# Kernel optimization log

Hardware: AMD Instinct MI355X
Metric: run time of the kernel (lower is better)

## Reference

```python
import jax, jax.numpy as jnp
import numpy as np

B, S, IN_DIM = 2, 2048, 1024
DIMS, QH, KVH = 1024, 16, 4
HD = DIMS // QH          # head_dims = 64
G = QH // KVH            # groups = 4


def setup_inputs() -> dict:
    key = jax.random.key(0)
    k1, k2, k3, k4, k5, k6 = jax.random.split(key, 6)
    scale = 0.02
    q_in = jax.random.normal(k1, (B, S, IN_DIM), dtype=jnp.float32)
    kv_in = jax.random.normal(k2, (B, S, IN_DIM), dtype=jnp.float32)
    # causal mask (True = attend)
    mask = jnp.tril(jnp.ones((S, S), dtype=bool))
    Wq = jax.random.normal(k3, (IN_DIM, QH, HD), dtype=jnp.float32) * scale
    Wk = jax.random.normal(k4, (IN_DIM, KVH, HD), dtype=jnp.float32) * scale
    Wv = jax.random.normal(k5, (IN_DIM, KVH, HD), dtype=jnp.float32) * scale
    Wo = jax.random.normal(k6, (KVH * HD, IN_DIM), dtype=jnp.float32) * scale
    return {"q_in": q_in, "kv_in": kv_in, "mask": mask,
            "Wq": Wq, "Wk": Wk, "Wv": Wv, "Wo": Wo}


def reference(q_in, kv_in, mask, Wq, Wk, Wv, Wo):
    b, s, _ = q_in.shape
    # projections (DenseGeneral, no bias)
    q = jnp.einsum('bsi,ihd->bshd', q_in, Wq)   # [B,S,QH,HD]
    k = jnp.einsum('bsi,ihd->bshd', kv_in, Wk)  # [B,S,KVH,HD]
    v = jnp.einsum('bsi,ihd->bshd', kv_in, Wv)  # [B,S,KVH,HD]
    # rearrange '... s (h g) d -> ... g h s d' with g=G (h outer, g inner),
    # then einsum '... g h s d, ... h a d -> ... h s a' sums over g.
    # Equivalent (and cheaper): sum q over the group axis first.
    q_g = q.reshape(b, s, KVH, G, HD).sum(axis=3)        # [B,S,KVH,HD]
    q_g = jnp.transpose(q_g, (0, 2, 1, 3))               # [B,KVH,S,HD]
    k = jnp.transpose(k, (0, 2, 1, 3))                   # [B,KVH,S,HD]
    v = jnp.transpose(v, (0, 2, 1, 3))                   # [B,KVH,S,HD]
    scores = jnp.einsum('bhsd,bhad->bhsa', q_g, k)       # [B,KVH,S,S]
    scores = jnp.where(mask[None, None, :, :], scores, -jnp.inf)
    attn = jax.nn.softmax(scores / (HD ** 0.5), axis=-1)
    out = jnp.einsum('bhsa,bhad->bhsd', attn, v)         # [B,KVH,S,HD]
    out = jnp.transpose(out, (0, 2, 1, 3)).reshape(b, s, KVH * HD)
    return out @ Wo                                      # [B,S,IN_DIM]
```

## Files before the change

kernel.cpp:

```cpp
#include <hip/hip_runtime.h>
#include <hip/hip_bf16.h>

#define SS 2048

typedef __attribute__((ext_vector_type(8))) short bf16x8;
typedef __attribute__((ext_vector_type(4))) float f32x4;

__device__ __forceinline__ short f2bf(float f){
    unsigned u = __float_as_uint(f);
    u += 0x7fff + ((u >> 16) & 1);
    return (short)(u >> 16);
}

__global__ __launch_bounds__(256) void k_prep_w(const float* __restrict__ Wq,
                                                const float* __restrict__ Wk,
                                                const float* __restrict__ Wv,
                                                const float* __restrict__ Wo,
                                                short* __restrict__ WcatT,
                                                short* __restrict__ WoT){
    __shared__ float Ts[64][65];
    const int bx = blockIdx.x;
    const int r  = threadIdx.x >> 2;
    const int cq = (threadIdx.x & 3) * 16;
    if (bx < 192) {
        const int ktile = bx & 15, ntile = bx >> 4;
        const int k0 = ktile * 64, n0 = ntile * 64;
        if (ntile < 4) {
            const float* base = Wq + (size_t)(k0 + r) * 1024 + ntile * 256;
            #pragma unroll
            for (int i = 0; i < 16; i += 4) {
                float4 a = *(const float4*)(base + cq + i);
                float4 b = *(const float4*)(base + 64 + cq + i);
                float4 c = *(const float4*)(base + 128 + cq + i);
                float4 d = *(const float4*)(base + 192 + cq + i);
                Ts[r][cq+i]   = 0.125f * (a.x + b.x + c.x + d.x);
                Ts[r][cq+i+1] = 0.125f * (a.y + b.y + c.y + d.y);
                Ts[r][cq+i+2] = 0.125f * (a.z + b.z + c.z + d.z);
                Ts[r][cq+i+3] = 0.125f * (a.w + b.w + c.w + d.w);
            }
        } else {
            const float* W = (ntile < 8) ? Wk : Wv;
            const float* base = W + (size_t)(k0 + r) * 256 + (ntile & 3) * 64;
            #pragma unroll
            for (int i = 0; i < 16; i += 4) {
                float4 a = *(const float4*)(base + cq + i);
                Ts[r][cq+i] = a.x; Ts[r][cq+i+1] = a.y;
                Ts[r][cq+i+2] = a.z; Ts[r][cq+i+3] = a.w;
            }
        }
        __syncthreads();
        short tmp[16];
        #pragma unroll
        for (int i = 0; i < 16; ++i) tmp[i] = f2bf(Ts[cq+i][r]);
        short* dst = WcatT + (size_t)(n0 + r) * 1024 + k0 + cq;
        *(bf16x8*)dst       = *(bf16x8*)&tmp[0];
        *(bf16x8*)(dst + 8) = *(bf16x8*)&tmp[8];
    } else {
        const int b2 = bx - 192;
        const int ktile = b2 & 3, ntile = b2 >> 2;
        const int k0 = ktile * 64, n0 = ntile * 64;
        const float* base = Wo + (size_t)(k0 + r) * 1024 + n0;
        #pragma unroll
        for (int i = 0; i < 16; i += 4) {
            float4 a = *(const float4*)(base + cq + i);
            Ts[r][cq+i] = a.x; Ts[r][cq+i+1] = a.y;
            Ts[r][cq+i+2] = a.z; Ts[r][cq+i+3] = a.w;
        }
        __syncthreads();
        short tmp[16];
        #pragma unroll
        for (int i = 0; i < 16; ++i) tmp[i] = f2bf(Ts[cq+i][r]);
        short* dst = WoT + (size_t)(n0 + r) * 256 + k0 + cq;
        *(bf16x8*)dst       = *(bf16x8*)&tmp[0];
        *(bf16x8*)(dst + 8) = *(bf16x8*)&tmp[8];
    }
}

__global__ __launch_bounds__(256) void k_gemm1(const float* __restrict__ q_in,
                                               const float* __restrict__ kv_in,
                                               const short* __restrict__ WcatT,
                                               short* __restrict__ pqk,
                                               short* __restrict__ vt){
    const int m0 = blockIdx.x * 128;
    const int n0 = blockIdx.y * 128;
    const float* X = (n0 < 256) ? q_in : kv_in;
    const int tid = threadIdx.x;
    const int wave = tid >> 6, lane = tid & 63, quad = lane >> 4, l16 = lane & 15;
    const int wrow = (wave & 1) * 64, wcol = (wave >> 1) * 64;
    const int r = tid >> 2, cc = (tid & 3) * 16;

    __shared__ short As[128][72];
    __shared__ short Bs[128][72];

    f32x4 acc[4][4];
    #pragma unroll
    for (int tm = 0; tm < 4; ++tm)
        #pragma unroll
        for (int tn = 0; tn < 4; ++tn) acc[tm][tn] = f32x4{0.f,0.f,0.f,0.f};

    short ta0[16], ta1[16];
    bf16x8 rb0, rb1, rb2, rb3;
    {
        const float* a0 = X + (size_t)(m0 + r) * 1024 + cc;
        const float* a1 = a0 + (size_t)64 * 1024;
        #pragma unroll
        for (int i = 0; i < 16; i += 4) {
            float4 f = *(const float4*)(a0 + i);
            ta0[i] = f2bf(f.x); ta0[i+1] = f2bf(f.y); ta0[i+2] = f2bf(f.z); ta0[i+3] = f2bf(f.w);
            float4 g = *(const float4*)(a1 + i);
            ta1[i] = f2bf(g.x); ta1[i+1] = f2bf(g.y); ta1[i+2] = f2bf(g.z); ta1[i+3] = f2bf(g.w);
        }
        const short* b0 = WcatT + (size_t)(n0 + r) * 1024 + cc;
        const short* b1 = b0 + (size_t)64 * 1024;
        rb0 = *(const bf16x8*)b0; rb1 = *(const bf16x8*)(b0 + 8);
        rb2 = *(const bf16x8*)b1; rb3 = *(const bf16x8*)(b1 + 8);
    }

    for (int k0 = 0; k0 < 1024; k0 += 64) {
        *(bf16x8*)&As[r][cc]          = *(bf16x8*)&ta0[0];
        *(bf16x8*)&As[r][cc + 8]      = *(bf16x8*)&ta0[8];
        *(bf16x8*)&As[r + 64][cc]     = *(bf16x8*)&ta1[0];
        *(bf16x8*)&As[r + 64][cc + 8] = *(bf16x8*)&ta1[8];
        *(bf16x8*)&Bs[r][cc]          = rb0;
        *(bf16x8*)&Bs[r][cc + 8]      = rb1;
        *(bf16x8*)&Bs[r + 64][cc]     = rb2;
        *(bf16x8*)&Bs[r + 64][cc + 8] = rb3;
        __syncthreads();
        if (k0 + 64 < 1024) {
            const float* a0 = X + (size_t)(m0 + r) * 1024 + k0 + 64 + cc;
            const float* a1 = a0 + (size_t)64 * 1024;
            #pragma unroll
            for (int i = 0; i < 16; i += 4) {
                float4 f = *(const float4*)(a0 + i);
                ta0[i] = f2bf(f.x); ta0[i+1] = f2bf(f.y); ta0[i+2] = f2bf(f.z); ta0[i+3] = f2bf(f.w);
                float4 g = *(const float4*)(a1 + i);
                ta1[i] = f2bf(g.x); ta1[i+1] = f2bf(g.y); ta1[i+2] = f2bf(g.z); ta1[i+3] = f2bf(g.w);
            }
            const short* b0 = WcatT + (size_t)(n0 + r) * 1024 + k0 + 64 + cc;
            const short* b1 = b0 + (size_t)64 * 1024;
            rb0 = *(const bf16x8*)b0; rb1 = *(const bf16x8*)(b0 + 8);
            rb2 = *(const bf16x8*)b1; rb3 = *(const bf16x8*)(b1 + 8);
        }
        #pragma unroll
        for (int ks = 0; ks < 2; ++ks) {
            bf16x8 a[4];
            #pragma unroll
            for (int tm = 0; tm < 4; ++tm)
                a[tm] = *(bf16x8*)&As[wrow + tm * 16 + l16][ks * 32 + quad * 8];
            #pragma unroll
            for (int tn = 0; tn < 4; ++tn) {
                bf16x8 b = *(bf16x8*)&Bs[wcol + tn * 16 + l16][ks * 32 + quad * 8];
                #pragma unroll
                for (int tm = 0; tm < 4; ++tm)
                    acc[tm][tn] = __builtin_amdgcn_mfma_f32_16x16x32_bf16(a[tm], b, acc[tm][tn], 0, 0, 0);
            }
        }
        __syncthreads();
    }
    if (n0 < 512) {
        #pragma unroll
        for (int tm = 0; tm < 4; ++tm) {
            const int mrow = m0 + wrow + tm * 16 + quad * 4;
            #pragma unroll
            for (int tn = 0; tn < 4; ++tn) {
                const int col = n0 + wcol + tn * 16 + l16;
                #pragma unroll
                for (int rg = 0; rg < 4; ++rg)
                    pqk[(size_t)(mrow + rg) * 512 + col] = f2bf(acc[tm][tn][rg]);
            }
        }
    } else {
        #pragma unroll
        for (int tm = 0; tm < 4; ++tm) {
            const int mrow = m0 + wrow + tm * 16 + quad * 4;
            #pragma unroll
            for (int tn = 0; tn < 4; ++tn) {
                const int colv = n0 - 512 + wcol + tn * 16 + l16;
                const int vh = colv >> 6, d = colv & 63;
                #pragma unroll
                for (int rg = 0; rg < 4; ++rg) {
                    int m = mrow + rg, batch = m >> 11, s = m & 2047;
                    vt[((size_t)((batch * 4 + vh) * 64 + d)) * 2048 + s] = f2bf(acc[tm][tn][rg]);
                }
            }
        }
    }
}

__global__ __launch_bounds__(256) void k_attn4(const short* __restrict__ pqk,
                                               const short* __restrict__ vt,
                                               float* __restrict__ Op,
                                               float* __restrict__ Lp,
                                               int nsplit){
    const int bx = blockIdx.x;
    const int qt = 31 - (bx / nsplit);
    const int s  = bx - (bx / nsplit) * nsplit;
    const int kv = blockIdx.y, batch = blockIdx.z;
    const int tid = threadIdx.x;
    const int wave = tid >> 6, lane = tid & 63, quad = lane >> 4, l16 = lane & 15;
    const int r = tid >> 2, c = (tid & 3) * 16;
    const int part = (((batch * 4 + kv) * 32 + qt) * nsplit + s);

    __shared__ short Ks[64][72];
    __shared__ short Vs[64][72];
    __shared__ short Ps[64][72];

    const size_t qrow = (size_t)(batch * SS + qt * 64 + wave * 16 + l16);
    bf16x8 aq0 = *(const bf16x8*)(pqk + qrow * 512 + kv * 64 + quad * 8);
    bf16x8 aq1 = *(const bf16x8*)(pqk + qrow * 512 + kv * 64 + 32 + quad * 8);

    f32x4 accO[4];
    #pragma unroll
    for (int t = 0; t < 4; ++t) accO[t] = f32x4{0.f, 0.f, 0.f, 0.f};
    float lrow[4] = {0.f, 0.f, 0.f, 0.f};

    bf16x8 rk0, rk1, rv0, rv1;
    int kt = s;
    if (kt <= qt) {
        const short* ksrc = pqk + (size_t)(batch * SS + kt * 64 + r) * 512 + 256 + kv * 64 + c;
        rk0 = *(const bf16x8*)ksrc; rk1 = *(const bf16x8*)(ksrc + 8);
        const short* vsrc = vt + ((size_t)((batch * 4 + kv) * 64 + r)) * 2048 + kt * 64 + c;
        rv0 = *(const bf16x8*)vsrc; rv1 = *(const bf16x8*)(vsrc + 8);
    }
    for (; kt <= qt; kt += nsplit) {
        *(bf16x8*)&Ks[r][c]     = rk0;
        *(bf16x8*)&Ks[r][c + 8] = rk1;
        *(bf16x8*)&Vs[r][c]     = rv0;
        *(bf16x8*)&Vs[r][c + 8] = rv1;
        __syncthreads();
        if (kt + nsplit <= qt) {
            const short* ksrc = pqk + (size_t)(batch * SS + (kt + nsplit) * 64 + r) * 512 + 256 + kv * 64 + c;
            rk0 = *(const bf16x8*)ksrc; rk1 = *(const bf16x8*)(ksrc + 8);
            const short* vsrc = vt + ((size_t)((batch * 4 + kv) * 64 + r)) * 2048 + (kt + nsplit) * 64 + c;
            rv0 = *(const bf16x8*)vsrc; rv1 = *(const bf16x8*)(vsrc + 8);
        }

        f32x4 sc[4];
        #pragma unroll
        for (int t = 0; t < 4; ++t) sc[t] = f32x4{0.f, 0.f, 0.f, 0.f};
        #pragma unroll
        for (int ks = 0; ks < 2; ++ks) {
            bf16x8 a = ks ? aq1 : aq0;
            #pragma unroll
            for (int t = 0; t < 4; ++t) {
                bf16x8 b = *(bf16x8*)&Ks[t * 16 + l16][ks * 32 + quad * 8];
                sc[t] = __builtin_amdgcn_mfma_f32_16x16x32_bf16(a, b, sc[t], 0, 0, 0);
            }
        }
        if (kt == qt) {
            #pragma unroll
            for (int t = 0; t < 4; ++t) {
                int colg = t * 16 + l16;
                #pragma unroll
                for (int rg = 0; rg < 4; ++rg)
                    if (colg > wave * 16 + quad * 4 + rg) sc[t][rg] = -1e30f;
            }
        }
        #pragma unroll
        for (int t = 0; t < 4; ++t) {
            #pragma unroll
            for (int rg = 0; rg < 4; ++rg) {
                float p = __expf(sc[t][rg]);
                lrow[rg] += p;
                Ps[wave * 16 + quad * 4 + rg][t * 16 + l16] = f2bf(p);
            }
        }
        #pragma unroll
        for (int ks = 0; ks < 2; ++ks) {
            bf16x8 ap = *(bf16x8*)&Ps[wave * 16 + l16][ks * 32 + quad * 8];
            #pragma unroll
            for (int t = 0; t < 4; ++t) {
                bf16x8 bv = *(bf16x8*)&Vs[t * 16 + l16][ks * 32 + quad * 8];
                accO[t] = __builtin_amdgcn_mfma_f32_16x16x32_bf16(ap, bv, accO[t], 0, 0, 0);
            }
        }
        __syncthreads();
    }
    #pragma unroll
    for (int rg = 0; rg < 4; ++rg) {
        float l = lrow[rg];
        l += __shfl_xor(l, 1);
        l += __shfl_xor(l, 2);
        l += __shfl_xor(l, 4);
        l += __shfl_xor(l, 8);
        lrow[rg] = l;
    }
    #pragma unroll
    for (int rg = 0; rg < 4; ++rg) {
        int row = wave * 16 + quad * 4 + rg;
        #pragma unroll
        for (int t = 0; t < 4; ++t)
            Op[(size_t)part * 4096 + row * 64 + t * 16 + l16] = accO[t][rg];
    }
    if (l16 == 0) {
        #pragma unroll
        for (int rg = 0; rg < 4; ++rg)
            Lp[part * 64 + (wave * 16 + quad * 4 + rg)] = lrow[rg];
    }
}

__global__ __launch_bounds__(256) void k_combine(const float* __restrict__ Op,
                                                 const float* __restrict__ Lp,
                                                 short* __restrict__ ao,
                                                 int nsplit){
    const int qt = blockIdx.x, kv = blockIdx.y, batch = blockIdx.z;
    const int tid = threadIdx.x;
    const int rr = tid >> 2, cs = (tid & 3) * 16;
    const int pbase = ((batch * 4 + kv) * 32 + qt) * nsplit;
    float lsum = 0.f;
    for (int i = 0; i < nsplit; ++i) lsum += Lp[(pbase + i) * 64 + rr];
    float inv = 1.f / lsum;
    float o[16];
    #pragma unroll
    for (int j = 0; j < 16; ++j) o[j] = 0.f;
    for (int i = 0; i < nsplit; ++i) {
        const float* src = Op + (size_t)(pbase + i) * 4096 + rr * 64 + cs;
        #pragma unroll
        for (int j = 0; j < 16; j += 4) {
            float4 f = *(const float4*)(src + j);
            o[j] += f.x; o[j+1] += f.y; o[j+2] += f.z; o[j+3] += f.w;
        }
    }
    short* dst = ao + (size_t)(batch * SS + qt * 64 + rr) * 256 + kv * 64 + cs;
    #pragma unroll
    for (int j = 0; j < 16; ++j)
        dst[j] = f2bf(o[j] * inv);
}

__global__ __launch_bounds__(256) void k_gemm2(const short* __restrict__ ao,
                                               const short* __restrict__ WoT,
                                               float* __restrict__ out){
    const int m0 = blockIdx.x * 128;
    const int n0 = blockIdx.y * 128;
    const int tid = threadIdx.x;
    const int wave = tid >> 6, lane = tid & 63, quad = lane >> 4, l16 = lane & 15;
    const int wrow = (wave & 1) * 64, wcol = (wave >> 1) * 64;
    const int r = tid >> 2, cc = (tid & 3) * 16;

    __shared__ short As[128][72];
    __shared__ short Bs[128][72];

    f32x4 acc[4][4];
    #pragma unroll
    for (int tm = 0; tm < 4; ++tm)
        #pragma unroll
        for (int tn = 0; tn < 4; ++tn) acc[tm][tn] = f32x4{0.f,0.f,0.f,0.f};

    bf16x8 ra0, ra1, ra2, ra3, rb0, rb1, rb2, rb3;
    {
        const short* a0 = ao + (size_t)(m0 + r) * 256 + cc;
        const short* a1 = a0 + (size_t)64 * 256;
        const short* b0 = WoT + (size_t)(n0 + r) * 256 + cc;
        const short* b1 = b0 + (size_t)64 * 256;
        ra0 = *(const bf16x8*)a0; ra1 = *(const bf16x8*)(a0 + 8);
        ra2 = *(const bf16x8*)a1; ra3 = *(const bf16x8*)(a1 + 8);
        rb0 = *(const bf16x8*)b0; rb1 = *(const bf16x8*)(b0 + 8);
        rb2 = *(const bf16x8*)b1; rb3 = *(const bf16x8*)(b1 + 8);
    }
    for (int k0 = 0; k0 < 256; k0 += 64) {
        *(bf16x8*)&As[r][cc]          = ra0;
        *(bf16x8*)&As[r][cc + 8]      = ra1;
        *(bf16x8*)&As[r + 64][cc]     = ra2;
        *(bf16x8*)&As[r + 64][cc + 8] = ra3;
        *(bf16x8*)&Bs[r][cc]          = rb0;
        *(bf16x8*)&Bs[r][cc + 8]      = rb1;
        *(bf16x8*)&Bs[r + 64][cc]     = rb2;
        *(bf16x8*)&Bs[r + 64][cc + 8] = rb3;
        __syncthreads();
        if (k0 + 64 < 256) {
            const short* a0 = ao + (size_t)(m0 + r) * 256 + k0 + 64 + cc;
            const short* a1 = a0 + (size_t)64 * 256;
            const short* b0 = WoT + (size_t)(n0 + r) * 256 + k0 + 64 + cc;
            const short* b1 = b0 + (size_t)64 * 256;
            ra0 = *(const bf16x8*)a0; ra1 = *(const bf16x8*)(a0 + 8);
            ra2 = *(const bf16x8*)a1; ra3 = *(const bf16x8*)(a1 + 8);
            rb0 = *(const bf16x8*)b0; rb1 = *(const bf16x8*)(b0 + 8);
            rb2 = *(const bf16x8*)b1; rb3 = *(const bf16x8*)(b1 + 8);
        }
        #pragma unroll
        for (int ks = 0; ks < 2; ++ks) {
            bf16x8 a[4];
            #pragma unroll
            for (int tm = 0; tm < 4; ++tm)
                a[tm] = *(bf16x8*)&As[wrow + tm * 16 + l16][ks * 32 + quad * 8];
            #pragma unroll
            for (int tn = 0; tn < 4; ++tn) {
                bf16x8 b = *(bf16x8*)&Bs[wcol + tn * 16 + l16][ks * 32 + quad * 8];
                #pragma unroll
                for (int tm = 0; tm < 4; ++tm)
                    acc[tm][tn] = __builtin_amdgcn_mfma_f32_16x16x32_bf16(a[tm], b, acc[tm][tn], 0, 0, 0);
            }
        }
        __syncthreads();
    }
    #pragma unroll
    for (int tm = 0; tm < 4; ++tm) {
        const int mrow = m0 + wrow + tm * 16 + quad * 4;
        #pragma unroll
        for (int tn = 0; tn < 4; ++tn) {
            const int col = n0 + wcol + tn * 16 + l16;
            #pragma unroll
            for (int rg = 0; rg < 4; ++rg)
                out[(size_t)(mrow + rg) * 1024 + col] = acc[tm][tn][rg];
        }
    }
}

extern "C" void kernel_launch(void* const* d_in, const int* in_sizes, int n_in,
                              void* d_out, int out_size, void* d_ws, size_t ws_size,
                              hipStream_t stream) {
    const float* q_in  = (const float*)d_in[0];
    const float* kv_in = (const float*)d_in[1];
    int wqi = 3;
    for (int i = 2; i < n_in; ++i)
        if (in_sizes[i] == 1024 * 16 * 64) { wqi = i; break; }
    const float* Wq = (const float*)d_in[wqi];
    const float* Wk = (const float*)d_in[wqi + 1];
    const float* Wv = (const float*)d_in[wqi + 2];
    const float* Wo = (const float*)d_in[wqi + 3];
    float* out = (float*)d_out;

    char* ws = (char*)d_ws;
    short* WcatT = (short*)(ws);
    short* WoT   = (short*)(ws + 1572864);
    short* ao    = (short*)(ws + 2097152);
    short* pqk   = (short*)(ws + 4194304);
    short* vt    = (short*)(ws + 8388608);
    float* Lp    = (float*)(ws + 10485760);
    float* Op    = (float*)(ws + 33554432);
    const int nsplit = 8;

    hipLaunchKernelGGL(k_prep_w,  dim3(256),     dim3(256), 0, stream,
                       Wq, Wk, Wv, Wo, WcatT, WoT);
    hipLaunchKernelGGL(k_gemm1,   dim3(32, 6),   dim3(256), 0, stream,
                       q_in, kv_in, WcatT, pqk, vt);
    hipLaunchKernelGGL(k_attn4,   dim3(32 * nsplit, 4, 2), dim3(256), 0, stream,
                       pqk, vt, Op, Lp, nsplit);
    hipLaunchKernelGGL(k_combine, dim3(32, 4, 2), dim3(256), 0, stream,
                       Op, Lp, ao, nsplit);
    hipLaunchKernelGGL(k_gemm2,   dim3(32, 8),   dim3(256), 0, stream,
                       ao, WoT, out);
}
```

Baseline: 161.2 us.

## Stage V transpose through shared memory and store split-K partials as bf16

The V epilogue of the first GEMM now transposes the tile through shared memory, so the vt writes become coalesced 16-byte stores instead of scattered 2-byte stores. The attention partial outputs are written as bf16 instead of fp32, which halves the traffic between the attention and combine kernels. The split count becomes a compile-time constant so the combine loops can be unrolled. Partial sums lose precision from the bf16 rounding, and the shared-memory buffer is merged so it can be reused for the transpose.

```diff
diff --git a/kernel.cpp b/kernel.cpp
--- a/kernel.cpp
+++ b/kernel.cpp
@@ -2,6 +2,7 @@
 #include <hip/hip_bf16.h>
 
 #define SS 2048
+#define NSPLIT 8
 
 typedef __attribute__((ext_vector_type(8))) short bf16x8;
 typedef __attribute__((ext_vector_type(4))) float f32x4;
@@ -10,6 +11,9 @@
     unsigned u = __float_as_uint(f);
     u += 0x7fff + ((u >> 16) & 1);
     return (short)(u >> 16);
+}
+__device__ __forceinline__ float bf2f(short s){
+    return __uint_as_float(((unsigned)(unsigned short)s) << 16);
 }
 
 __global__ __launch_bounds__(256) void k_prep_w(const float* __restrict__ Wq,
@@ -76,6 +80,8 @@
     }
 }
 
+#define AS(r, c) SMEM[(r) * 72 + (c)]
+#define BS(r, c) SMEM[128 * 72 + (r) * 72 + (c)]
 __global__ __launch_bounds__(256) void k_gemm1(const float* __restrict__ q_in,
                                                const float* __restrict__ kv_in,
                                                const short* __restrict__ WcatT,
@@ -89,8 +95,7 @@
     const int wrow = (wave & 1) * 64, wcol = (wave >> 1) * 64;
     const int r = tid >> 2, cc = (tid & 3) * 16;
 
-    __shared__ short As[128][72];
-    __shared__ short Bs[128][72];
+    __shared__ short SMEM[2 * 128 * 72];
 
     f32x4 acc[4][4];
     #pragma unroll
@@ -117,14 +122,14 @@
     }
 
     for (int k0 = 0; k0 < 1024; k0 += 64) {
-        *(bf16x8*)&As[r][cc]          = *(bf16x8*)&ta0[0];
-        *(bf16x8*)&As[r][cc + 8]      = *(bf16x8*)&ta0[8];
-        *(bf16x8*)&As[r + 64][cc]     = *(bf16x8*)&ta1[0];
-        *(bf16x8*)&As[r + 64][cc + 8] = *(bf16x8*)&ta1[8];
-        *(bf16x8*)&Bs[r][cc]          = rb0;
-        *(bf16x8*)&Bs[r][cc + 8]      = rb1;
-        *(bf16x8*)&Bs[r + 64][cc]     = rb2;
-        *(bf16x8*)&Bs[r + 64][cc + 8] = rb3;
+        *(bf16x8*)&AS(r, cc)          = *(bf16x8*)&ta0[0];
+        *(bf16x8*)&AS(r, cc + 8)      = *(bf16x8*)&ta0[8];
+        *(bf16x8*)&AS(r + 64, cc)     = *(bf16x8*)&ta1[0];
+        *(bf16x8*)&AS(r + 64, cc + 8) = *(bf16x8*)&ta1[8];
+        *(bf16x8*)&BS(r, cc)          = rb0;
+        *(bf16x8*)&BS(r, cc + 8)      = rb1;
+        *(bf16x8*)&BS(r + 64, cc)     = rb2;
+        *(bf16x8*)&BS(r + 64, cc + 8) = rb3;
         __syncthreads();
         if (k0 + 64 < 1024) {
             const float* a0 = X + (size_t)(m0 + r) * 1024 + k0 + 64 + cc;
@@ -146,10 +151,10 @@
             bf16x8 a[4];
             #pragma unroll
             for (int tm = 0; tm < 4; ++tm)
-                a[tm] = *(bf16x8*)&As[wrow + tm * 16 + l16][ks * 32 + quad * 8];
+                a[tm] = *(bf16x8*)&AS(wrow + tm * 16 + l16, ks * 32 + quad * 8);
             #pragma unroll
             for (int tn = 0; tn < 4; ++tn) {
-                bf16x8 b = *(bf16x8*)&Bs[wcol + tn * 16 + l16][ks * 32 + quad * 8];
+                bf16x8 b = *(bf16x8*)&BS(wcol + tn * 16 + l16, ks * 32 + quad * 8);
                 #pragma unroll
                 for (int tm = 0; tm < 4; ++tm)
                     acc[tm][tn] = __builtin_amdgcn_mfma_f32_16x16x32_bf16(a[tm], b, acc[tm][tn], 0, 0, 0);
@@ -172,34 +177,42 @@
     } else {
         #pragma unroll
         for (int tm = 0; tm < 4; ++tm) {
-            const int mrow = m0 + wrow + tm * 16 + quad * 4;
+            const int ml = wrow + tm * 16 + quad * 4;
             #pragma unroll
             for (int tn = 0; tn < 4; ++tn) {
-                const int colv = n0 - 512 + wcol + tn * 16 + l16;
-                const int vh = colv >> 6, d = colv & 63;
+                const int cl = wcol + tn * 16 + l16;
                 #pragma unroll
-                for (int rg = 0; rg < 4; ++rg) {
-                    int m = mrow + rg, batch = m >> 11, s = m & 2047;
-                    vt[((size_t)((batch * 4 + vh) * 64 + d)) * 2048 + s] = f2bf(acc[tm][tn][rg]);
-                }
-            }
-        }
+                for (int rg = 0; rg < 4; ++rg)
+                    SMEM[cl * 136 + ml + rg] = f2bf(acc[tm][tn][rg]);
+            }
+        }
+        __syncthreads();
+        const int row  = tid >> 1;
+        const int half = tid & 1;
+        const int colv = (n0 - 512) + row;
+        const int vh = colv >> 6, d = colv & 63;
+        const int batch = m0 >> 11;
+        const int s0 = (m0 & 2047) + half * 64;
+        short* dst = vt + ((size_t)((batch * 4 + vh) * 64 + d)) * 2048 + s0;
+        const short* src = &SMEM[row * 136 + half * 64];
+        #pragma unroll
+        for (int i = 0; i < 64; i += 8)
+            *(bf16x8*)(dst + i) = *(const bf16x8*)(src + i);
     }
 }
 
 __global__ __launch_bounds__(256) void k_attn4(const short* __restrict__ pqk,
                                                const short* __restrict__ vt,
-                                               float* __restrict__ Op,
-                                               float* __restrict__ Lp,
-                                               int nsplit){
+                                               short* __restrict__ Op,
+                                               float* __restrict__ Lp){
     const int bx = blockIdx.x;
-    const int qt = 31 - (bx / nsplit);
-    const int s  = bx - (bx / nsplit) * nsplit;
+    const int qt = 31 - (bx / NSPLIT);
+    const int s  = bx - (bx / NSPLIT) * NSPLIT;
     const int kv = blockIdx.y, batch = blockIdx.z;
     const int tid = threadIdx.x;
     const int wave = tid >> 6, lane = tid & 63, quad = lane >> 4, l16 = lane & 15;
     const int r = tid >> 2, c = (tid & 3) * 16;
-    const int part = (((batch * 4 + kv) * 32 + qt) * nsplit + s);
+    const int part = (((batch * 4 + kv) * 32 + qt) * NSPLIT + s);
 
     __shared__ short Ks[64][72];
     __shared__ short Vs[64][72];
@@ -222,16 +235,16 @@
         const short* vsrc = vt + ((size_t)((batch * 4 + kv) * 64 + r)) * 2048 + kt * 64 + c;
         rv0 = *(const bf16x8*)vsrc; rv1 = *(const bf16x8*)(vsrc + 8);
     }
-    for (; kt <= qt; kt += nsplit) {
+    for (; kt <= qt; kt += NSPLIT) {
         *(bf16x8*)&Ks[r][c]     = rk0;
         *(bf16x8*)&Ks[r][c + 8] = rk1;
         *(bf16x8*)&Vs[r][c]     = rv0;
         *(bf16x8*)&Vs[r][c + 8] = rv1;
         __syncthreads();
-        if (kt + nsplit <= qt) {
-            const short* ksrc = pqk + (size_t)(batch * SS + (kt + nsplit) * 64 + r) * 512 + 256 + kv * 64 + c;
+        if (kt + NSPLIT <= qt) {
+            const short* ksrc = pqk + (size_t)(batch * SS + (kt + NSPLIT) * 64 + r) * 512 + 256 + kv * 64 + c;
             rk0 = *(const bf16x8*)ksrc; rk1 = *(const bf16x8*)(ksrc + 8);
-            const short* vsrc = vt + ((size_t)((batch * 4 + kv) * 64 + r)) * 2048 + (kt + nsplit) * 64 + c;
+            const short* vsrc = vt + ((size_t)((batch * 4 + kv) * 64 + r)) * 2048 + (kt + NSPLIT) * 64 + c;
             rv0 = *(const bf16x8*)vsrc; rv1 = *(const bf16x8*)(vsrc + 8);
         }
 
@@ -290,7 +303,7 @@
         int row = wave * 16 + quad * 4 + rg;
         #pragma unroll
         for (int t = 0; t < 4; ++t)
-            Op[(size_t)part * 4096 + row * 64 + t * 16 + l16] = accO[t][rg];
+            Op[(size_t)part * 4096 + row * 64 + t * 16 + l16] = f2bf(accO[t][rg]);
     }
     if (l16 == 0) {
         #pragma unroll
@@ -299,27 +312,27 @@
     }
 }
 
-__global__ __launch_bounds__(256) void k_combine(const float* __restrict__ Op,
+__global__ __launch_bounds__(256) void k_combine(const short* __restrict__ Op,
                                                  const float* __restrict__ Lp,
-                                                 short* __restrict__ ao,
-                                                 int nsplit){
+                                                 short* __restrict__ ao){
     const int qt = blockIdx.x, kv = blockIdx.y, batch = blockIdx.z;
     const int tid = threadIdx.x;
     const int rr = tid >> 2, cs = (tid & 3) * 16;
-    const int pbase = ((batch * 4 + kv) * 32 + qt) * nsplit;
+    const int pbase = ((batch * 4 + kv) * 32 + qt) * NSPLIT;
     float lsum = 0.f;
-    for (int i = 0; i < nsplit; ++i) lsum += Lp[(pbase + i) * 64 + rr];
+    #pragma unroll
+    for (int i = 0; i < NSPLIT; ++i) lsum += Lp[(pbase + i) * 64 + rr];
     float inv = 1.f / lsum;
     float o[16];
     #pragma unroll
     for (int j = 0; j < 16; ++j) o[j] = 0.f;
-    for (int i = 0; i < nsplit; ++i) {
-        const float* src = Op + (size_t)(pbase + i) * 4096 + rr * 64 + cs;
-        #pragma unroll
-        for (int j = 0; j < 16; j += 4) {
-            float4 f = *(const float4*)(src + j);
-            o[j] += f.x; o[j+1] += f.y; o[j+2] += f.z; o[j+3] += f.w;
-        }
+    #pragma unroll
+    for (int i = 0; i < NSPLIT; ++i) {
+        const short* src = Op + (size_t)(pbase + i) * 4096 + rr * 64 + cs;
+        bf16x8 v0 = *(const bf16x8*)src;
+        bf16x8 v1 = *(const bf16x8*)(src + 8);
+        #pragma unroll
+        for (int j = 0; j < 8; ++j) { o[j] += bf2f(v0[j]); o[j + 8] += bf2f(v1[j]); }
     }
     short* dst = ao + (size_t)(batch * SS + qt * 64 + rr) * 256 + kv * 64 + cs;
     #pragma unroll
@@ -427,17 +440,16 @@
     short* pqk   = (short*)(ws + 4194304);
     short* vt    = (short*)(ws + 8388608);
     float* Lp    = (float*)(ws + 10485760);
-    float* Op    = (float*)(ws + 33554432);
-    const int nsplit = 8;
+    short* Op    = (short*)(ws + 33554432);
 
     hipLaunchKernelGGL(k_prep_w,  dim3(256),     dim3(256), 0, stream,
                        Wq, Wk, Wv, Wo, WcatT, WoT);
     hipLaunchKernelGGL(k_gemm1,   dim3(32, 6),   dim3(256), 0, stream,
                        q_in, kv_in, WcatT, pqk, vt);
-    hipLaunchKernelGGL(k_attn4,   dim3(32 * nsplit, 4, 2), dim3(256), 0, stream,
-                       pqk, vt, Op, Lp, nsplit);
+    hipLaunchKernelGGL(k_attn4,   dim3(32 * NSPLIT, 4, 2), dim3(256), 0, stream,
+                       pqk, vt, Op, Lp);
     hipLaunchKernelGGL(k_combine, dim3(32, 4, 2), dim3(256), 0, stream,
-                       Op, Lp, ao, nsplit);
+                       Op, Lp, ao);
     hipLaunchKernelGGL(k_gemm2,   dim3(32, 8),   dim3(256), 0, stream,
                        ao, WoT, out);
 }
```

Measured after the change: 158.8 us. About the same (-1.5%).
